# Kernel optimization log

Measured on AMD Instinct MI355X. Metric: run time of the kernel, lower is better.

Reference implementation:

```python
import jax, jax.numpy as jnp
import numpy as np

C = 256          # in_channels
CI = 128         # inter_channels = C // reduction
N_B, H, W = 4, 64, 64


def setup_inputs() -> dict:
    key = jax.random.key(0)
    ks = jax.random.split(key, 9)
    std = 0.01
    inp = {
        "x": jax.random.normal(ks[0], (N_B, C, H, W), dtype=jnp.float32),
        # 1x1 conv weights stored as [out_ch, in_ch]
        "w_g": jax.random.normal(ks[1], (CI, C), dtype=jnp.float32) * std,
        "b_g": jnp.zeros((CI,), dtype=jnp.float32),
        "w_theta": jax.random.normal(ks[2], (CI, C), dtype=jnp.float32) * std,
        "b_theta": jnp.zeros((CI,), dtype=jnp.float32),
        "w_phi": jax.random.normal(ks[3], (CI, C), dtype=jnp.float32) * std,
        "b_phi": jnp.zeros((CI,), dtype=jnp.float32),
        # conv_out: use small random instead of exact zeros so output is non-trivial
        "w_out": jax.random.normal(ks[4], (C, CI), dtype=jnp.float32) * std,
        "b_out": jnp.zeros((C,), dtype=jnp.float32),
    }
    return inp


def reference(x, w_g, b_g, w_theta, b_theta, w_phi, b_phi, w_out, b_out):
    n, c, h, w = x.shape
    nhw = h * w
    xf = x.reshape(n, c, nhw)                                   # [n, C, N]
    # 1x1 convs == channel matmuls
    g_x = jnp.einsum('ncs,oc->nso', xf, w_g) + b_g              # [n, N, CI]
    theta_x = jnp.einsum('ncs,oc->nso', xf, w_theta) + b_theta  # [n, N, CI]
    phi_x = jnp.einsum('ncs,oc->nos', xf, w_phi) + b_phi[None, :, None]  # [n, CI, N]
    # pairwise weights: [n, N, N]
    pw = jnp.einsum('nqc,ncs->nqs', theta_x, phi_x)
    # faithful to original: DIVIDE by d**-0.5 (i.e. multiply by sqrt(d))
    pw = pw / (theta_x.shape[-1] ** (-0.5))
    pw = jax.nn.softmax(pw, axis=-1)
    y = jnp.einsum('nqs,nsc->nqc', pw, g_x)                     # [n, N, CI]
    y = y.transpose(0, 2, 1).reshape(n, -1, h, w)               # [n, CI, H, W]
    out = jnp.einsum('nchw,oc->nohw', y, w_out) + b_out[None, :, None, None]
    return x + out
```

## Files before the change

kernel.cpp:

```cpp
#include <hip/hip_runtime.h>
#include <cmath>

typedef __attribute__((ext_vector_type(8))) short bf16x8;
typedef __attribute__((ext_vector_type(4))) float f32x4;

#define MFMA16(a,b,c)  __builtin_amdgcn_mfma_f32_16x16x32_bf16((a),(b),(c),0,0,0)

#if __has_builtin(__builtin_amdgcn_exp2f)
#define EXP2F(x) __builtin_amdgcn_exp2f(x)
#else
#define EXP2F(x) exp2f(x)
#endif

#define KSCALE 16.3222312f

#define NB 4
#define CH 256
#define CI 128
#define NS 4096

__device__ __forceinline__ unsigned short f2bf(float f) {
    unsigned int u = __builtin_bit_cast(unsigned int, f);
    u += 0x7fffu + ((u >> 16) & 1u);
    return (unsigned short)(u >> 16);
}
__device__ __forceinline__ unsigned int pk2(float lo, float hi) {
    return (unsigned int)f2bf(lo) | ((unsigned int)f2bf(hi) << 16);
}
__device__ __forceinline__ unsigned int pk2t(float lo, float hi) {
    unsigned int ul = __builtin_bit_cast(unsigned int, lo);
    unsigned int uh = __builtin_bit_cast(unsigned int, hi);
    return (uh & 0xffff0000u) | (ul >> 16);
}
__device__ __forceinline__ float bf2f(unsigned int ush) {
    return __builtin_bit_cast(float, ush << 16);
}

__device__ __forceinline__ void gload16(void* lds, const void* g) {
    __builtin_amdgcn_global_load_lds(
        (const __attribute__((address_space(1))) unsigned int*)g,
        (__attribute__((address_space(3))) unsigned int*)lds,
        16, 0, 0);
}

__global__ void wcvt_kernel(const float* __restrict__ w_g, const float* __restrict__ w_th,
                            const float* __restrict__ w_ph, const float* __restrict__ w_out,
                            const float* __restrict__ b_g, const float* __restrict__ b_th,
                            const float* __restrict__ b_ph,
                            unsigned short* __restrict__ wbf, float* __restrict__ bsc) {
    int i = blockIdx.x * 256 + threadIdx.x;
    float v;
    if (i < 32768)        v = w_g[i];
    else if (i < 65536)   v = w_th[i - 32768] * KSCALE;
    else if (i < 98304)   v = w_ph[i - 65536];
    else                  v = w_out[i - 98304];
    wbf[i] = f2bf(v);
    if (i < 128)          bsc[i] = b_g[i];
    else if (i < 256)     bsc[i] = b_th[i - 128] * KSCALE;
    else if (i < 384)     bsc[i] = b_ph[i - 256];
}

__global__ __launch_bounds__(512, 2)
void proj_kernel(const float* __restrict__ x,
                 const unsigned short* __restrict__ wbf, const float* __restrict__ bsc,
                 unsigned short* __restrict__ theta,
                 unsigned short* __restrict__ phi,
                 unsigned short* __restrict__ gT) {
    const int tid  = threadIdx.x;
    const int wid  = tid >> 6;
    const int lane = tid & 63;
    const int quad = lane >> 4;
    const int l15  = lane & 15;
    const int stile = blockIdx.x;
    const int n     = blockIdx.y;
    const int s0    = stile * 64;

    const float* xN = x + (size_t)n * CH * NS;

    __shared__ unsigned int xp[64 * 128];

#pragma unroll
    for (int i = 0; i < 4; i++) {
        int t  = i * 512 + tid;
        int s4 = t & 15;
        int cp = t >> 4;
        const float* p0 = xN + (size_t)(2 * cp) * NS + s0 + s4 * 4;
        float4 a = *(const float4*)p0;
        float4 b = *(const float4*)(p0 + NS);
        int col = (((cp >> 2) ^ (s4 & 7)) << 2) | (cp & 3);
        unsigned int* xr = xp + (s4 * 4) * 128 + col;
        xr[0]   = pk2(a.x, b.x);
        xr[128] = pk2(a.y, b.y);
        xr[256] = pk2(a.z, b.z);
        xr[384] = pk2(a.w, b.w);
    }
    __syncthreads();

    const int srow = (wid & 3) * 16 + l15;
    const int oh   = wid >> 2;
    const int sw7  = (srow >> 2) & 7;
#pragma unroll
    for (int wi = 0; wi < 3; wi++) {
        f32x4 acc[4];
#pragma unroll
        for (int ot = 0; ot < 4; ot++) acc[ot] = (f32x4){0.f, 0.f, 0.f, 0.f};
        const unsigned short* W = wbf + (size_t)wi * 32768 + (size_t)oh * 64 * CH;
#pragma unroll
        for (int kc = 0; kc < 8; kc++) {
            bf16x8 af = *(const bf16x8*)(&xp[srow * 128 + (((kc * 4 + quad) ^ sw7) << 2)]);
#pragma unroll
            for (int ot = 0; ot < 4; ot++) {
                bf16x8 wf = *(const bf16x8*)(W + (size_t)(ot * 16 + l15) * CH + kc * 32 + quad * 8);
                acc[ot] = MFMA16(af, wf, acc[ot]);
            }
        }
        const float* Bv = bsc + wi * 128 + oh * 64;
#pragma unroll
        for (int ot = 0; ot < 4; ot++) {
            int o = oh * 64 + ot * 16 + l15;
            float bias = Bv[ot * 16 + l15];
#pragma unroll
            for (int r = 0; r < 4; r++) {
                int sg = s0 + (wid & 3) * 16 + quad * 4 + r;
                float v = acc[ot][r] + bias;
                if (wi == 0)
                    gT[((size_t)n * CI + o) * NS + sg] = f2bf(v);
                else if (wi == 1)
                    theta[((size_t)n * NS + sg) * CI + o] = f2bf(v);
                else
                    phi[((size_t)n * NS + sg) * CI + o] = f2bf(v);
            }
        }
    }
}

__global__ __launch_bounds__(256, 2)
void attn_kernel(const unsigned short* __restrict__ theta,
                 const unsigned short* __restrict__ phi,
                 const unsigned short* __restrict__ gT,
                 unsigned short* __restrict__ Opart,
                 float* __restrict__ lbuf) {
    const int tid  = threadIdx.x;
    const int wid  = tid >> 6;
    const int lane = tid & 63;
    const int quad = lane >> 4;
    const int l15  = lane & 15;
    const int sn    = blockIdx.x;
    const int split = sn >> 2;
    const int n     = sn & 3;
    const int qb    = blockIdx.y;
    const int qbase = qb * 128 + wid * 32;

    const unsigned short* thN = theta + (size_t)n * NS * CI;
    const unsigned short* phN = phi   + (size_t)n * NS * CI;
    const unsigned short* gN  = gT    + (size_t)n * CI * NS;

    __shared__ unsigned short smem[40960];
    unsigned short* Kb = smem;
    unsigned short* Vb = smem + 16384;
    unsigned short* Plds = smem + 32768;

    bf16x8 qf[2][4];
#pragma unroll
    for (int qt = 0; qt < 2; qt++)
#pragma unroll
        for (int kc = 0; kc < 4; kc++)
            qf[qt][kc] = *(const bf16x8*)(thN + (size_t)(qbase + qt * 16 + l15) * CI + kc * 32 + quad * 8);

    f32x4 O[8][2];
#pragma unroll
    for (int ct = 0; ct < 8; ct++)
#pragma unroll
        for (int qt = 0; qt < 2; qt++) O[ct][qt] = (f32x4){0.f, 0.f, 0.f, 0.f};
    float lrun[2] = {0.f, 0.f};

    const int sbase0 = split * 1024;
    const int lh16 = lane >> 4, lm16 = lane & 15;
    const int lh8  = lane >> 3, lm8  = lane & 7;

#pragma unroll
    for (int i = 0; i < 4; i++) {
        int seg = wid * 4 + i;
        int s   = seg * 4 + lh16;
        int j   = lm16 ^ (s & 15);
        gload16(Kb + seg * 512, phN + (size_t)(sbase0 + s) * CI + j * 8);
    }
#pragma unroll
    for (int i = 0; i < 4; i++) {
        int seg = wid * 4 + i;
        int c   = seg * 8 + lh8;
        int j   = lm8 ^ (c & 7);
        gload16(Vb + seg * 512, gN + (size_t)c * NS + sbase0 + j * 8);
    }

    for (int ck = 0; ck < 16; ck++) {
        const int cur = ck & 1, nxt = cur ^ 1;
        unsigned short* Kc = Kb + cur * 8192;
        unsigned short* Vc = Vb + cur * 8192;
        __syncthreads();

        if (ck + 1 < 16) {
            const int sb1 = sbase0 + (ck + 1) * 64;
#pragma unroll
            for (int i = 0; i < 4; i++) {
                int seg = wid * 4 + i;
                int s   = seg * 4 + lh16;
                int j   = lm16 ^ (s & 15);
                gload16(Kb + nxt * 8192 + seg * 512, phN + (size_t)(sb1 + s) * CI + j * 8);
            }
#pragma unroll
            for (int i = 0; i < 4; i++) {
                int seg = wid * 4 + i;
                int c   = seg * 8 + lh8;
                int j   = lm8 ^ (c & 7);
                gload16(Vb + nxt * 8192 + seg * 512, gN + (size_t)c * NS + sb1 + j * 8);
            }
        }

        f32x4 S[2][4];
#pragma unroll
        for (int qt = 0; qt < 2; qt++)
#pragma unroll
            for (int st = 0; st < 4; st++) S[qt][st] = (f32x4){0.f, 0.f, 0.f, 0.f};
#pragma unroll
        for (int st = 0; st < 4; st++) {
#pragma unroll
            for (int kc = 0; kc < 4; kc++) {
                int s = st * 16 + l15;
                bf16x8 kf = *(const bf16x8*)(Kc + s * 128 + ((kc * 4 + quad) ^ l15) * 8);
#pragma unroll
                for (int qt = 0; qt < 2; qt++)
                    S[qt][st] = MFMA16(kf, qf[qt][kc], S[qt][st]);
            }
        }

#pragma unroll
        for (int qt = 0; qt < 2; qt++) {
            float rsl = 0.f;
            unsigned int u[8];
#pragma unroll
            for (int st = 0; st < 4; st++) {
                float p0 = EXP2F(S[qt][st][0]);
                float p1 = EXP2F(S[qt][st][1]);
                float p2 = EXP2F(S[qt][st][2]);
                float p3 = EXP2F(S[qt][st][3]);
                rsl += (p0 + p1) + (p2 + p3);
                u[st * 2]     = pk2t(p0, p1);
                u[st * 2 + 1] = pk2t(p2, p3);
            }
            lrun[qt] += rsl;
            unsigned short* Pw = Plds + (wid * 2 + qt) * 1024 + l15 * 64 + (quad & 1) * 4;
#pragma unroll
            for (int st = 0; st < 4; st++) {
                int p = ((st * 2 + (quad >> 1)) ^ (l15 & 7)) * 8;
                *(uint2*)(Pw + p) = make_uint2(u[st * 2], u[st * 2 + 1]);
            }
        }

#pragma unroll
        for (int kc2 = 0; kc2 < 2; kc2++) {
            bf16x8 pf[2];
#pragma unroll
            for (int qt = 0; qt < 2; qt++)
                pf[qt] = *(const bf16x8*)(Plds + (wid * 2 + qt) * 1024 + l15 * 64 + (((kc2 * 4 + quad) ^ (l15 & 7)) * 8));
#pragma unroll
            for (int ct = 0; ct < 8; ct++) {
                bf16x8 vf = *(const bf16x8*)(Vc + (ct * 16 + l15) * 64 + (((kc2 * 4 + quad) ^ (l15 & 7)) * 8));
#pragma unroll
                for (int qt = 0; qt < 2; qt++)
                    O[ct][qt] = MFMA16(vf, pf[qt], O[ct][qt]);
            }
        }
    }

    __syncthreads();
    float* tb = (float*)smem + wid * 2048;
    const size_t obase = ((size_t)(split * NB + n)) * NS * CI;
#pragma unroll
    for (int qt = 0; qt < 2; qt++) {
#pragma unroll
        for (int ct = 0; ct < 8; ct++) {
            int p = (ct * 4 + quad) ^ l15;
            *(f32x4*)(tb + l15 * 128 + p * 4) = O[ct][qt];
        }
#pragma unroll
        for (int i = 0; i < 4; i++) {
            int flat = i * 64 + lane;
            int row = flat >> 4, jj = flat & 15;
            f32x4 a = *(const f32x4*)(tb + row * 128 + ((jj * 2) ^ row) * 4);
            f32x4 b = *(const f32x4*)(tb + row * 128 + ((jj * 2 + 1) ^ row) * 4);
            int q = qbase + qt * 16 + row;
            uint4 pkv;
            pkv.x = pk2(a[0], a[1]); pkv.y = pk2(a[2], a[3]);
            pkv.z = pk2(b[0], b[1]); pkv.w = pk2(b[2], b[3]);
            *(uint4*)(Opart + obase + (size_t)q * CI + jj * 8) = pkv;
        }
    }
    lrun[0] += __shfl_xor(lrun[0], 16); lrun[0] += __shfl_xor(lrun[0], 32);
    lrun[1] += __shfl_xor(lrun[1], 16); lrun[1] += __shfl_xor(lrun[1], 32);
    if (quad == 0) {
#pragma unroll
        for (int qt = 0; qt < 2; qt++) {
            int q = qbase + qt * 16 + l15;
            lbuf[(split * NB + n) * NS + q] = lrun[qt];
        }
    }
}

__global__ __launch_bounds__(256, 4)
void outproj_kernel(const float* __restrict__ x,
                    const unsigned short* __restrict__ wbf,
                    const float* __restrict__ b_out,
                    const unsigned short* __restrict__ Opart,
                    const float* __restrict__ lbuf,
                    float* __restrict__ out) {
    const int tid  = threadIdx.x;
    const int wid  = tid >> 6;
    const int lane = tid & 63;
    const int quad = lane >> 4;
    const int l15  = lane & 15;
    const int oh = blockIdx.y;
    const int n  = blockIdx.z;
    const int sw = blockIdx.x * 64 + wid * 16;
    const int T  = NB * NS;

    const int srow = n * NS + sw + l15;
    float l = 0.f;
#pragma unroll
    for (int k = 0; k < 4; k++) l += lbuf[k * T + srow];
    float rinv = 1.0f / l;

    bf16x8 yb[4];
#pragma unroll
    for (int kc = 0; kc < 4; kc++) {
        float f0 = 0.f, f1 = 0.f, f2 = 0.f, f3 = 0.f;
        float f4 = 0.f, f5 = 0.f, f6 = 0.f, f7 = 0.f;
#pragma unroll
        for (int k = 0; k < 4; k++) {
            uint4 v = *(const uint4*)(Opart + ((size_t)k * T + srow) * CI + kc * 32 + quad * 8);
            f0 += bf2f(v.x & 0xffffu); f1 += bf2f(v.x >> 16);
            f2 += bf2f(v.y & 0xffffu); f3 += bf2f(v.y >> 16);
            f4 += bf2f(v.z & 0xffffu); f5 += bf2f(v.z >> 16);
            f6 += bf2f(v.w & 0xffffu); f7 += bf2f(v.w >> 16);
        }
        union { unsigned int uu[4]; bf16x8 vv; } r;
        r.uu[0] = pk2(f0 * rinv, f1 * rinv);
        r.uu[1] = pk2(f2 * rinv, f3 * rinv);
        r.uu[2] = pk2(f4 * rinv, f5 * rinv);
        r.uu[3] = pk2(f6 * rinv, f7 * rinv);
        yb[kc] = r.vv;
    }

    const unsigned short* wob = wbf + 3 * 32768 + (size_t)oh * 128 * CI;
    f32x4 acc[8];
#pragma unroll
    for (int ot = 0; ot < 8; ot++) acc[ot] = (f32x4){0.f, 0.f, 0.f, 0.f};
#pragma unroll
    for (int kc = 0; kc < 4; kc++) {
#pragma unroll
        for (int ot = 0; ot < 8; ot++) {
            bf16x8 wa = *(const bf16x8*)(wob + (size_t)(ot * 16 + l15) * CI + kc * 32 + quad * 8);
            acc[ot] = MFMA16(wa, yb[kc], acc[ot]);
        }
    }
#pragma unroll
    for (int ot = 0; ot < 8; ot++) {
#pragma unroll
        for (int r = 0; r < 4; r++) {
            int o = oh * 128 + ot * 16 + quad * 4 + r;
            size_t idx = ((size_t)n * CH + o) * NS + sw + l15;
            out[idx] = x[idx] + acc[ot][r] + b_out[o];
        }
    }
}

extern "C" void kernel_launch(void* const* d_in, const int* in_sizes, int n_in,
                              void* d_out, int out_size, void* d_ws, size_t ws_size,
                              hipStream_t stream) {
    const float* x     = (const float*)d_in[0];
    const float* w_g   = (const float*)d_in[1];
    const float* b_g   = (const float*)d_in[2];
    const float* w_th  = (const float*)d_in[3];
    const float* b_th  = (const float*)d_in[4];
    const float* w_ph  = (const float*)d_in[5];
    const float* b_ph  = (const float*)d_in[6];
    const float* w_out = (const float*)d_in[7];
    const float* b_out = (const float*)d_in[8];
    float* out = (float*)d_out;

    char* ws = (char*)d_ws;
    unsigned short* theta = (unsigned short*)(ws + 0);
    unsigned short* phi   = (unsigned short*)(ws + 4194304);
    unsigned short* gT    = (unsigned short*)(ws + 8388608);
    unsigned short* Opart = (unsigned short*)(ws + 12582912);
    float* lbuf  = (float*)(ws + 29360128);
    unsigned short* wbf = (unsigned short*)(ws + 29622272);
    float* bsc   = (float*)(ws + 29884416);

    wcvt_kernel<<<512, 256, 0, stream>>>(w_g, w_th, w_ph, w_out, b_g, b_th, b_ph, wbf, bsc);
    proj_kernel<<<dim3(64, NB), 512, 0, stream>>>(x, wbf, bsc, theta, phi, gT);
    attn_kernel<<<dim3(16, 32), 256, 0, stream>>>(theta, phi, gT, Opart, lbuf);
    outproj_kernel<<<dim3(64, 2, NB), 256, 0, stream>>>(x, wbf, b_out, Opart, lbuf, out);
}
```

Before: 162.8 us.

## Feed softmax P directly from registers into 16x16x16 MFMA, dropping LDS round-trip

Measured after the change: 167.7 us. +3.0%, slower.

```diff
diff --git a/kernel.cpp b/kernel.cpp
--- a/kernel.cpp
+++ b/kernel.cpp
@@ -2,9 +2,11 @@
 #include <cmath>
 
 typedef __attribute__((ext_vector_type(8))) short bf16x8;
+typedef __attribute__((ext_vector_type(4))) short bf16x4;
 typedef __attribute__((ext_vector_type(4))) float f32x4;
 
 #define MFMA16(a,b,c)  __builtin_amdgcn_mfma_f32_16x16x32_bf16((a),(b),(c),0,0,0)
+#define MFMA16K16(a,b,c) __builtin_amdgcn_mfma_f32_16x16x16bf16_1k((a),(b),(c),0,0,0)
 
 #if __has_builtin(__builtin_amdgcn_exp2f)
 #define EXP2F(x) __builtin_amdgcn_exp2f(x)
@@ -155,10 +157,9 @@
     const unsigned short* phN = phi   + (size_t)n * NS * CI;
     const unsigned short* gN  = gT    + (size_t)n * CI * NS;
 
-    __shared__ unsigned short smem[40960];
+    __shared__ unsigned short smem[32768];
     unsigned short* Kb = smem;
     unsigned short* Vb = smem + 16384;
-    unsigned short* Plds = smem + 32768;
 
     bf16x8 qf[2][4];
 #pragma unroll
@@ -222,6 +223,7 @@
         for (int qt = 0; qt < 2; qt++)
 #pragma unroll
             for (int st = 0; st < 4; st++) S[qt][st] = (f32x4){0.f, 0.f, 0.f, 0.f};
+        __builtin_amdgcn_s_setprio(1);
 #pragma unroll
         for (int st = 0; st < 4; st++) {
 #pragma unroll
@@ -233,11 +235,12 @@
                     S[qt][st] = MFMA16(kf, qf[qt][kc], S[qt][st]);
             }
         }
-
+        __builtin_amdgcn_s_setprio(0);
+
+        bf16x4 pa[2][4];
 #pragma unroll
         for (int qt = 0; qt < 2; qt++) {
             float rsl = 0.f;
-            unsigned int u[8];
 #pragma unroll
             for (int st = 0; st < 4; st++) {
                 float p0 = EXP2F(S[qt][st][0]);
@@ -245,32 +248,28 @@
                 float p2 = EXP2F(S[qt][st][2]);
                 float p3 = EXP2F(S[qt][st][3]);
                 rsl += (p0 + p1) + (p2 + p3);
-                u[st * 2]     = pk2t(p0, p1);
-                u[st * 2 + 1] = pk2t(p2, p3);
+                union { unsigned int uu[2]; bf16x4 v; } pkv;
+                pkv.uu[0] = pk2t(p0, p1);
+                pkv.uu[1] = pk2t(p2, p3);
+                pa[qt][st] = pkv.v;
             }
             lrun[qt] += rsl;
-            unsigned short* Pw = Plds + (wid * 2 + qt) * 1024 + l15 * 64 + (quad & 1) * 4;
-#pragma unroll
-            for (int st = 0; st < 4; st++) {
-                int p = ((st * 2 + (quad >> 1)) ^ (l15 & 7)) * 8;
-                *(uint2*)(Pw + p) = make_uint2(u[st * 2], u[st * 2 + 1]);
-            }
-        }
-
-#pragma unroll
-        for (int kc2 = 0; kc2 < 2; kc2++) {
-            bf16x8 pf[2];
-#pragma unroll
-            for (int qt = 0; qt < 2; qt++)
-                pf[qt] = *(const bf16x8*)(Plds + (wid * 2 + qt) * 1024 + l15 * 64 + (((kc2 * 4 + quad) ^ (l15 & 7)) * 8));
+        }
+
+        __builtin_amdgcn_s_setprio(1);
+#pragma unroll
+        for (int st = 0; st < 4; st++) {
+            const int g = (st * 2 + (quad >> 1)) ^ (l15 & 7);
+            const int so = g * 8 + (quad & 1) * 4;
 #pragma unroll
             for (int ct = 0; ct < 8; ct++) {
-                bf16x8 vf = *(const bf16x8*)(Vc + (ct * 16 + l15) * 64 + (((kc2 * 4 + quad) ^ (l15 & 7)) * 8));
+                bf16x4 vf = *(const bf16x4*)(Vc + (ct * 16 + l15) * 64 + so);
 #pragma unroll
                 for (int qt = 0; qt < 2; qt++)
-                    O[ct][qt] = MFMA16(vf, pf[qt], O[ct][qt]);
-            }
-        }
+                    O[ct][qt] = MFMA16K16(vf, pa[qt][st], O[ct][qt]);
+            }
+        }
+        __builtin_amdgcn_s_setprio(0);
     }
 
     __syncthreads();
@@ -295,6 +294,7 @@
             pkv.z = pk2(b[0], b[1]); pkv.w = pk2(b[2], b[3]);
             *(uint4*)(Opart + obase + (size_t)q * CI + jj * 8) = pkv;
         }
+        __syncthreads();
     }
     lrun[0] += __shfl_xor(lrun[0], 16); lrun[0] += __shfl_xor(lrun[0], 32);
     lrun[1] += __shfl_xor(lrun[1], 16); lrun[1] += __shfl_xor(lrun[1], 32);
```
